# Optimization experiments

Hardware: AMD Instinct MI355X
Metric: run time of the kernel (lower is better)

The kernel has to match this reference:

```python
import jax, jax.numpy as jnp
import numpy as np

B, CIN, COUT, H, W = 2, 64, 64, 64, 2048
EPS = 1e-5


def unfold3(x):
    # x: [B, C, H, W] -> [B, H*W, 9, C], torch.nn.Unfold(k=3, pad=1) layout
    b, c, h, w = x.shape
    xp = jnp.pad(x, ((0, 0), (0, 0), (1, 1), (1, 1)))
    # kernel positions in row-major (ki, kj) order; index 4 is the center
    patches = jnp.stack([xp[:, :, i:i + h, j:j + w]
                         for i in range(3) for j in range(3)], axis=2)  # [B,C,9,H,W]
    return patches.reshape(b, c, 9, h * w).transpose(0, 3, 2, 1)  # [B,HW,9,C]


def setup_inputs() -> dict:
    key = jax.random.key(0)
    ks = jax.random.split(key, 8)
    x = jax.random.normal(ks[0], (B, 3 + CIN, H, W), dtype=jnp.float32)
    mask = jax.random.randint(ks[1], (B, 1, H, W), 0, 2, dtype=jnp.int32)
    w_spatial = jax.random.normal(ks[2], (CIN, 4), dtype=jnp.float32) * 0.5
    b_spatial = jax.random.normal(ks[3], (CIN,), dtype=jnp.float32) * 0.1
    w_channel = jax.random.normal(ks[4], (CIN, 4), dtype=jnp.float32) * 0.5
    b_channel = jax.random.normal(ks[5], (CIN,), dtype=jnp.float32) * 0.1
    w_agg = jax.random.normal(ks[6], (COUT, 9 * CIN), dtype=jnp.float32) * (1.0 / np.sqrt(9 * CIN))
    gamma = jnp.ones((COUT,), dtype=jnp.float32)
    beta = jnp.zeros((COUT,), dtype=jnp.float32)
    return {"x": x, "mask": mask, "w_spatial": w_spatial, "b_spatial": b_spatial,
            "w_channel": w_channel, "b_channel": b_channel, "w_agg": w_agg,
            "gamma": gamma, "beta": beta}


def reference(x, mask, w_spatial, b_spatial, w_channel, b_channel, w_agg, gamma, beta):
    b, _, h, w = x.shape
    x_un = unfold3(x)                              # [B,HW,9,3+C]
    feat = x_un[..., 3:]                           # [B,HW,9,C]
    x_pn = x_un[..., :3]                           # [B,HW,9,3]
    m_un = unfold3(mask.astype(jnp.float32))       # [B,HW,9,1]

    rng = jnp.linalg.norm(x_pn, axis=-1, keepdims=True)
    x_pn4 = jnp.concatenate([x_pn, rng], axis=-1)  # [B,HW,9,4]
    pn_p0 = x_pn4 - x_pn4[:, :, 4:5, :]            # relative to 3x3 center

    ws = jnp.einsum('bnkm,cm->bnkc', pn_p0, w_spatial) + b_spatial
    wc = jnp.einsum('bnkm,cm->bnkc', pn_p0, w_channel) + b_channel
    ws = jnp.max(ws, axis=3, keepdims=True)        # [B,HW,9,1]
    wc = jnp.max(wc, axis=2, keepdims=True)        # [B,HW,1,C]
    ws = jax.nn.softmax(ws, axis=2)
    wc = jax.nn.softmax(wc, axis=3)
    weights = (ws + wc) * m_un                     # [B,HW,9,C]

    feat = (weights * feat).reshape(b, h * w, 9 * CIN)
    out = jnp.einsum('bnf,of->bno', feat, w_agg)   # [B,HW,COUT]
    out = out.transpose(0, 2, 1)                   # [B,COUT,HW]

    # BatchNorm1d in training mode: stats over (batch, spatial) per channel
    mu = jnp.mean(out, axis=(0, 2), keepdims=True)
    var = jnp.mean((out - mu) ** 2, axis=(0, 2), keepdims=True)
    out = (out - mu) * jax.lax.rsqrt(var + EPS)
    out = out * gamma[None, :, None] + beta[None, :, None]
    out = jax.nn.relu(out)
    return out.reshape(b, COUT, h, w)              # Fold(k=1) == reshape
```

## Files before the change

### kernel.cpp

```cpp
#include <hip/hip_runtime.h>
#include <math.h>
#include <cstddef>

#define HDIM 64
#define WDIM 2048
#define HW   (HDIM*WDIM)
#define BATCH 2
#define CIN  64
#define COUT 64
#define XC   (3+CIN)
#define NPIX (BATCH*HW)
#define NBLK (NPIX/64)
#define NB2  (NBLK*2)
#define EPS  1e-5f

typedef short  short8  __attribute__((ext_vector_type(8)));
typedef float  f32x16  __attribute__((ext_vector_type(16)));

__device__ __forceinline__ unsigned short f2bf(float f) {
    unsigned int u = __float_as_uint(f);
    u += 0x7fff + ((u >> 16) & 1);
    return (unsigned short)(u >> 16);
}

struct __align__(16) SmemA {
    float wsm[9][64];
    float mk[9][64];
    float winv[64];
    float wc[64][64];
    union {
        struct { unsigned short A[64][72];
                 unsigned short V[64][72]; } mm;
        float wspart[9][4][64];
    } u;
};

__global__ __launch_bounds__(256, 4)
void kernelA(const float* __restrict__ x, const int* __restrict__ mask,
             const float* __restrict__ w_sp, const float* __restrict__ b_sp,
             const float* __restrict__ w_ch, const float* __restrict__ b_ch,
             const float* __restrict__ w_agg,
             float* __restrict__ out, float* __restrict__ psum, float* __restrict__ psq)
{
    __shared__ SmemA s;
    const int tid = threadIdx.x;
    const int bid = blockIdx.x;
    const int b  = bid >> 11;
    const int r  = bid & 2047;
    const int h  = r >> 5;
    const int w0 = (r & 31) << 6;

    const int px = tid & 63;
    const int q  = tid >> 6;

    float p[9][4];
    float mkr[9];
    {
        const int wpix = w0 + px;
        #pragma unroll
        for (int k = 0; k < 9; ++k) {
            int hh = h + k/3 - 1;
            int ww = wpix + k%3 - 1;
            bool in = (hh >= 0) && (hh < HDIM) && (ww >= 0) && (ww < WDIM);
            float p0=0.f, p1=0.f, p2=0.f, mv=0.f;
            if (in) {
                size_t base = ((size_t)(b*XC)*HDIM + hh)*(size_t)WDIM + ww;
                p0 = x[base];
                p1 = x[base + (size_t)HW];
                p2 = x[base + 2*(size_t)HW];
                mv = (float)mask[((size_t)b*HDIM + hh)*(size_t)WDIM + ww];
            }
            p[k][0]=p0; p[k][1]=p1; p[k][2]=p2;
            p[k][3]=sqrtf(p0*p0 + p1*p1 + p2*p2);
            mkr[k]=mv;
        }
        float c0=p[4][0], c1=p[4][1], c2=p[4][2], c3=p[4][3];
        #pragma unroll
        for (int k = 0; k < 9; ++k) {
            p[k][0]-=c0; p[k][1]-=c1; p[k][2]-=c2; p[k][3]-=c3;
        }
    }

    float wsp[9];
    #pragma unroll
    for (int k=0;k<9;++k) wsp[k] = -1e30f;
    for (int cc = 0; cc < 16; ++cc) {
        int c = q*16 + cc;
        float a0=w_sp[c*4+0], a1=w_sp[c*4+1], a2=w_sp[c*4+2], a3=w_sp[c*4+3], bs=b_sp[c];
        float d0=w_ch[c*4+0], d1=w_ch[c*4+1], d2=w_ch[c*4+2], d3=w_ch[c*4+3], bc=b_ch[c];
        float tmax = -1e30f;
        #pragma unroll
        for (int k=0;k<9;++k) {
            float sv = fmaf(p[k][0],a0, fmaf(p[k][1],a1, fmaf(p[k][2],a2, fmaf(p[k][3],a3, bs))));
            wsp[k] = fmaxf(wsp[k], sv);
            float tv = fmaf(p[k][0],d0, fmaf(p[k][1],d1, fmaf(p[k][2],d2, fmaf(p[k][3],d3, bc))));
            tmax = fmaxf(tmax, tv);
        }
        s.wc[c][px] = tmax;
    }
    #pragma unroll
    for (int k=0;k<9;++k) s.u.wspart[k][q][px] = wsp[k];
    __syncthreads();

    if (q == 0) {
        float v[9]; float mx = -1e30f;
        #pragma unroll
        for (int k=0;k<9;++k) {
            float a = s.u.wspart[k][0][px];
            a = fmaxf(a, s.u.wspart[k][1][px]);
            a = fmaxf(a, s.u.wspart[k][2][px]);
            a = fmaxf(a, s.u.wspart[k][3][px]);
            v[k]=a; mx=fmaxf(mx,a);
        }
        float sum=0.f;
        #pragma unroll
        for (int k=0;k<9;++k) { v[k]=__expf(v[k]-mx); sum+=v[k]; }
        float inv = 1.0f/sum;
        #pragma unroll
        for (int k=0;k<9;++k) {
            s.wsm[k][px] = v[k]*inv*mkr[k];
            s.mk[k][px]  = mkr[k];
        }
    } else if (q == 1) {
        float mx=-1e30f;
        for (int c=0;c<64;++c) mx = fmaxf(mx, s.wc[c][px]);
        float sum=0.f;
        for (int c=0;c<64;++c) {
            float e = __expf(s.wc[c][px]-mx);
            s.wc[c][px] = e;
            sum += e;
        }
        s.winv[px] = 1.0f/sum;
    }
    __syncthreads();

    const int lane = tid & 63;
    const int wv   = tid >> 6;
    const int mrow = lane & 31;
    const int half = lane >> 5;
    const int co0  = (wv & 1) * 32;
    const int px0  = (wv >> 1) * 32;

    f32x16 acc;
    #pragma unroll
    for (int i=0;i<16;++i) acc[i]=0.f;

    for (int kk = 0; kk < 9; ++kk) {
        #pragma unroll
        for (int i=0;i<4;++i) {
            int idx4 = tid + i*256;
            int co = idx4 >> 4;
            int k4 = idx4 & 15;
            float4 t = *(const float4*)(w_agg + (size_t)co*576 + kk*64 + k4*4);
            unsigned long long pk =  (unsigned long long)f2bf(t.x)
                                  | ((unsigned long long)f2bf(t.y)<<16)
                                  | ((unsigned long long)f2bf(t.z)<<32)
                                  | ((unsigned long long)f2bf(t.w)<<48);
            *(unsigned long long*)&s.u.mm.A[co][k4*4] = pk;
        }
        {
            int di = kk/3 - 1, dj = (kk%3) - 1;
            int hh = h + di;
            int ww = w0 + px + dj;
            bool inb = (hh>=0) && (hh<HDIM) && (ww>=0) && (ww<WDIM);
            int hhc = hh<0?0:(hh>HDIM-1?HDIM-1:hh);
            int wwc = ww<0?0:(ww>WDIM-1?WDIM-1:ww);
            const float* xb = x + ((size_t)(b*XC + 3)*HDIM + hhc)*(size_t)WDIM + wwc;
            float a_k = s.wsm[kk][px];
            float m2  = s.mk[kk][px] * s.winv[px];
            unsigned short vv[16];
            #pragma unroll
            for (int j=0;j<16;++j) {
                int c = 16*q + j;
                float f = inb ? xb[(size_t)c*HW] : 0.f;
                vv[j] = f2bf(fmaf(m2, s.wc[c][px], a_k) * f);
            }
            unsigned short* vp = &s.u.mm.V[px][16*q];
            short8 lo, hi;
            #pragma unroll
            for (int j=0;j<8;++j) { lo[j]=(short)vv[j]; hi[j]=(short)vv[8+j]; }
            *(short8*)vp       = lo;
            *(short8*)(vp + 8) = hi;
        }
        __syncthreads();
        #pragma unroll
        for (int ks=0; ks<4; ++ks) {
            short8 af = *(const short8*)&s.u.mm.A[co0+mrow][ks*16 + half*8];
            short8 bf = *(const short8*)&s.u.mm.V[px0+mrow][ks*16 + half*8];
            acc = __builtin_amdgcn_mfma_f32_32x32x16_bf16(af, bf, acc, 0, 0, 0);
        }
        __syncthreads();
    }

    const int pxg = w0 + px0 + mrow;
    #pragma unroll
    for (int reg=0; reg<16; ++reg) {
        int row = (reg&3) + 8*(reg>>2) + 4*half;
        int co  = co0 + row;
        float v = acc[reg];
        out[((size_t)(b*COUT+co))*HW + (size_t)h*WDIM + pxg] = v;
        float s1 = v, s2 = v*v;
        #pragma unroll
        for (int m=1; m<32; m<<=1) {
            s1 += __shfl_xor(s1, m, 64);
            s2 += __shfl_xor(s2, m, 64);
        }
        if (mrow == 0) {
            psum[(size_t)co*NB2 + bid*2 + (wv>>1)] = s1;
            psq [(size_t)co*NB2 + bid*2 + (wv>>1)] = s2;
        }
    }
}

__global__ __launch_bounds__(256)
void kernelB(const float* __restrict__ psum, const float* __restrict__ psq,
             float* __restrict__ stats)
{
    int co = blockIdx.x;
    int tid = threadIdx.x;
    float s=0.f, sq=0.f;
    for (int j = tid; j < NB2; j += 256) {
        s  += psum[(size_t)co*NB2 + j];
        sq += psq [(size_t)co*NB2 + j];
    }
    #pragma unroll
    for (int m=1; m<64; m<<=1) { s += __shfl_xor(s,m,64); sq += __shfl_xor(sq,m,64); }
    __shared__ float rs[4], rq[4];
    int wv = tid>>6;
    if ((tid&63)==0){ rs[wv]=s; rq[wv]=sq; }
    __syncthreads();
    if (tid==0) {
        float S = rs[0]+rs[1]+rs[2]+rs[3];
        float Q = rq[0]+rq[1]+rq[2]+rq[3];
        float mu = S / (float)NPIX;
        float var = Q/(float)NPIX - mu*mu;
        stats[co]      = mu;
        stats[64+co]   = rsqrtf(var + EPS);
    }
}

__global__ __launch_bounds__(256)
void kernelC(float* __restrict__ out, const float* __restrict__ stats,
             const float* __restrict__ gamma, const float* __restrict__ beta)
{
    size_t idx4 = (size_t)blockIdx.x*256 + threadIdx.x;
    size_t flat = idx4*4;
    int co = (int)((flat >> 17) & 63);
    float mu = stats[co], rstd = stats[64+co];
    float g  = gamma[co]*rstd;
    float bb = fmaf(-mu, g, beta[co]);
    float4 v = *(float4*)(out + flat);
    v.x = fmaxf(fmaf(v.x, g, bb), 0.f);
    v.y = fmaxf(fmaf(v.y, g, bb), 0.f);
    v.z = fmaxf(fmaf(v.z, g, bb), 0.f);
    v.w = fmaxf(fmaf(v.w, g, bb), 0.f);
    *(float4*)(out + flat) = v;
}

extern "C" void kernel_launch(void* const* d_in, const int* in_sizes, int n_in,
                              void* d_out, int out_size, void* d_ws, size_t ws_size,
                              hipStream_t stream)
{
    const float* x     = (const float*)d_in[0];
    const int*   mask  = (const int*)  d_in[1];
    const float* w_sp  = (const float*)d_in[2];
    const float* b_sp  = (const float*)d_in[3];
    const float* w_ch  = (const float*)d_in[4];
    const float* b_ch  = (const float*)d_in[5];
    const float* w_agg = (const float*)d_in[6];
    const float* gamma = (const float*)d_in[7];
    const float* beta  = (const float*)d_in[8];
    float* out  = (float*)d_out;
    float* psum = (float*)d_ws;
    float* psq  = psum + (size_t)COUT*NB2;
    float* stats= psq  + (size_t)COUT*NB2;

    kernelA<<<NBLK, 256, 0, stream>>>(x, mask, w_sp, b_sp, w_ch, b_ch, w_agg, out, psum, psq);
    kernelB<<<COUT, 256, 0, stream>>>(psum, psq, stats);
    int grid_c = (NPIX*COUT/4)/256;
    kernelC<<<grid_c, 256, 0, stream>>>(out, stats, gamma, beta);
}
```

Before: 288.8 us.

## Pre-convert aggregation weights to bf16 and load MFMA A fragments from global memory

A small pre-kernel converts w_agg to bf16 once per call, replacing the per-block, per-tap fp32 load, convert and LDS staging of the A matrix. kernelA now loads A fragments straight from global memory into registers, which shrinks shared memory (possibly raising occupancy). The center tap is skipped in the spatial/channel weight loop since its relative position is zero, reducing it to the bias. kernelC processes 8 floats per thread instead of 4. The cost is an extra launch plus per-wave global loads of weights that are likely L2-resident.

```diff
diff --git a/kernel.cpp b/kernel.cpp
--- a/kernel.cpp
+++ b/kernel.cpp
@@ -29,17 +29,28 @@
     float winv[64];
     float wc[64][64];
     union {
-        struct { unsigned short A[64][72];
-                 unsigned short V[64][72]; } mm;
+        unsigned short V[64][72];
         float wspart[9][4][64];
     } u;
 };
+
+__global__ __launch_bounds__(256)
+void kernelW(const float* __restrict__ w_agg, unsigned short* __restrict__ wbf)
+{
+    int i = blockIdx.x*256 + threadIdx.x;
+    float4 t = ((const float4*)w_agg)[i];
+    unsigned long long pk =  (unsigned long long)f2bf(t.x)
+                          | ((unsigned long long)f2bf(t.y)<<16)
+                          | ((unsigned long long)f2bf(t.z)<<32)
+                          | ((unsigned long long)f2bf(t.w)<<48);
+    *(unsigned long long*)(wbf + (size_t)i*4) = pk;
+}
 
 __global__ __launch_bounds__(256, 4)
 void kernelA(const float* __restrict__ x, const int* __restrict__ mask,
              const float* __restrict__ w_sp, const float* __restrict__ b_sp,
              const float* __restrict__ w_ch, const float* __restrict__ b_ch,
-             const float* __restrict__ w_agg,
+             const unsigned short* __restrict__ wbf,
              float* __restrict__ out, float* __restrict__ psum, float* __restrict__ psq)
 {
     __shared__ SmemA s;
@@ -88,9 +99,11 @@
         int c = q*16 + cc;
         float a0=w_sp[c*4+0], a1=w_sp[c*4+1], a2=w_sp[c*4+2], a3=w_sp[c*4+3], bs=b_sp[c];
         float d0=w_ch[c*4+0], d1=w_ch[c*4+1], d2=w_ch[c*4+2], d3=w_ch[c*4+3], bc=b_ch[c];
-        float tmax = -1e30f;
+        float tmax = bc;
+        wsp[4] = fmaxf(wsp[4], bs);
         #pragma unroll
         for (int k=0;k<9;++k) {
+            if (k == 4) continue;
             float sv = fmaf(p[k][0],a0, fmaf(p[k][1],a1, fmaf(p[k][2],a2, fmaf(p[k][3],a3, bs))));
             wsp[k] = fmaxf(wsp[k], sv);
             float tv = fmaf(p[k][0],d0, fmaf(p[k][1],d1, fmaf(p[k][2],d2, fmaf(p[k][3],d3, bc))));
@@ -141,23 +154,18 @@
     const int co0  = (wv & 1) * 32;
     const int px0  = (wv >> 1) * 32;
 
+    const unsigned short* abase = wbf + (size_t)(co0+mrow)*576 + half*8;
+
     f32x16 acc;
     #pragma unroll
     for (int i=0;i<16;++i) acc[i]=0.f;
 
     for (int kk = 0; kk < 9; ++kk) {
-        #pragma unroll
-        for (int i=0;i<4;++i) {
-            int idx4 = tid + i*256;
-            int co = idx4 >> 4;
-            int k4 = idx4 & 15;
-            float4 t = *(const float4*)(w_agg + (size_t)co*576 + kk*64 + k4*4);
-            unsigned long long pk =  (unsigned long long)f2bf(t.x)
-                                  | ((unsigned long long)f2bf(t.y)<<16)
-                                  | ((unsigned long long)f2bf(t.z)<<32)
-                                  | ((unsigned long long)f2bf(t.w)<<48);
-            *(unsigned long long*)&s.u.mm.A[co][k4*4] = pk;
-        }
+        short8 af[4];
+        #pragma unroll
+        for (int ks=0; ks<4; ++ks)
+            af[ks] = *(const short8*)(abase + kk*64 + ks*16);
+
         {
             int di = kk/3 - 1, dj = (kk%3) - 1;
             int hh = h + di;
@@ -171,11 +179,11 @@
             unsigned short vv[16];
             #pragma unroll
             for (int j=0;j<16;++j) {
-                int c = 16*q + j;
+                unsigned c = 16u*q + j;
                 float f = inb ? xb[(size_t)c*HW] : 0.f;
                 vv[j] = f2bf(fmaf(m2, s.wc[c][px], a_k) * f);
             }
-            unsigned short* vp = &s.u.mm.V[px][16*q];
+            unsigned short* vp = &s.u.V[px][16*q];
             short8 lo, hi;
             #pragma unroll
             for (int j=0;j<8;++j) { lo[j]=(short)vv[j]; hi[j]=(short)vv[8+j]; }
@@ -185,9 +193,8 @@
         __syncthreads();
         #pragma unroll
         for (int ks=0; ks<4; ++ks) {
-            short8 af = *(const short8*)&s.u.mm.A[co0+mrow][ks*16 + half*8];
-            short8 bf = *(const short8*)&s.u.mm.V[px0+mrow][ks*16 + half*8];
-            acc = __builtin_amdgcn_mfma_f32_32x32x16_bf16(af, bf, acc, 0, 0, 0);
+            short8 bf = *(const short8*)&s.u.V[px0+mrow][ks*16 + half*8];
+            acc = __builtin_amdgcn_mfma_f32_32x32x16_bf16(af[ks], bf, acc, 0, 0, 0);
         }
         __syncthreads();
     }
@@ -243,18 +250,21 @@
 void kernelC(float* __restrict__ out, const float* __restrict__ stats,
              const float* __restrict__ gamma, const float* __restrict__ beta)
 {
-    size_t idx4 = (size_t)blockIdx.x*256 + threadIdx.x;
-    size_t flat = idx4*4;
+    size_t idx8 = (size_t)blockIdx.x*256 + threadIdx.x;
+    size_t flat = idx8*8;
     int co = (int)((flat >> 17) & 63);
     float mu = stats[co], rstd = stats[64+co];
     float g  = gamma[co]*rstd;
     float bb = fmaf(-mu, g, beta[co]);
-    float4 v = *(float4*)(out + flat);
-    v.x = fmaxf(fmaf(v.x, g, bb), 0.f);
-    v.y = fmaxf(fmaf(v.y, g, bb), 0.f);
-    v.z = fmaxf(fmaf(v.z, g, bb), 0.f);
-    v.w = fmaxf(fmaf(v.w, g, bb), 0.f);
-    *(float4*)(out + flat) = v;
+    #pragma unroll
+    for (int t=0;t<2;++t) {
+        float4 v = *(float4*)(out + flat + t*4);
+        v.x = fmaxf(fmaf(v.x, g, bb), 0.f);
+        v.y = fmaxf(fmaf(v.y, g, bb), 0.f);
+        v.z = fmaxf(fmaf(v.z, g, bb), 0.f);
+        v.w = fmaxf(fmaf(v.w, g, bb), 0.f);
+        *(float4*)(out + flat + t*4) = v;
+    }
 }
 
 extern "C" void kernel_launch(void* const* d_in, const int* in_sizes, int n_in,
@@ -274,9 +284,11 @@
     float* psum = (float*)d_ws;
     float* psq  = psum + (size_t)COUT*NB2;
     float* stats= psq  + (size_t)COUT*NB2;
-
-    kernelA<<<NBLK, 256, 0, stream>>>(x, mask, w_sp, b_sp, w_ch, b_ch, w_agg, out, psum, psq);
+    unsigned short* wbf = (unsigned short*)(stats + 128);
+
+    kernelW<<<36, 256, 0, stream>>>(w_agg, wbf);
+    kernelA<<<NBLK, 256, 0, stream>>>(x, mask, w_sp, b_sp, w_ch, b_ch, wbf, out, psum, psq);
     kernelB<<<COUT, 256, 0, stream>>>(psum, psq, stats);
-    int grid_c = (NPIX*COUT/4)/256;
+    int grid_c = (NPIX*COUT/8)/256;
     kernelC<<<grid_c, 256, 0, stream>>>(out, stats, gamma, beta);
 }
```

Measured after the change: 296.6 us. 1.03x slower.
